# Performance work log

Measured on AMD Instinct MI355X. Metric: run time of the kernel, lower is better.

The kernel has to match this reference:

```python
import jax, jax.numpy as jnp
import numpy as np

D_MODEL = 1024
N_HEADS = 16
D_FF = 4 * D_MODEL
CTX = 2048
EPS = 1e-5


def setup_inputs() -> dict:
    key = jax.random.key(0)
    ks = jax.random.split(key, 8)
    s = 0.02
    z = jax.random.normal(ks[0], (2, CTX, D_MODEL), dtype=jnp.float32)
    W_Q = jax.random.normal(ks[1], (D_MODEL, D_MODEL), dtype=jnp.float32) * s
    W_K = jax.random.normal(ks[2], (D_MODEL, D_MODEL), dtype=jnp.float32) * s
    W_V = jax.random.normal(ks[3], (D_MODEL, D_MODEL), dtype=jnp.float32) * s
    W_O = jax.random.normal(ks[4], (D_MODEL, D_MODEL), dtype=jnp.float32) * s
    W_fc = jax.random.normal(ks[5], (D_MODEL, D_FF), dtype=jnp.float32) * s
    W_proj = jax.random.normal(ks[6], (D_FF, D_MODEL), dtype=jnp.float32) * s
    g1 = jnp.ones((D_MODEL,), dtype=jnp.float32)
    g2 = jnp.ones((D_MODEL,), dtype=jnp.float32)
    return {"z": z, "W_Q": W_Q, "W_K": W_K, "W_V": W_V, "W_O": W_O,
            "W_fc": W_fc, "W_proj": W_proj, "g1": g1, "g2": g2}


def rmsnorm(x, gain):
    rms = jnp.sqrt(jnp.sum(x * x, axis=-1, keepdims=True) / x.shape[-1] + EPS)
    return (x / rms) * gain


def gelu_erf(x):
    return x * 0.5 * (1.0 + jax.lax.erf(x / jnp.sqrt(2.0).astype(x.dtype)))


def attention(zn, W_Q, W_K, W_V, W_O):
    B, T, D = zn.shape
    H = N_HEADS
    dh = D // H
    # [B,T,D] -> [B,H,T,dh]
    def split(x):
        return x.reshape(B, T, H, dh).transpose(0, 2, 1, 3)
    Q = split(zn @ W_Q)
    K = split(zn @ W_K)
    V = split(zn @ W_V)
    scores = jnp.einsum('bhtd,bhsd->bhts', Q, K) / jnp.sqrt(jnp.float32(dh))
    causal = jnp.triu(jnp.ones((T, T), dtype=bool), k=1)  # True above diagonal -> masked
    scores = jnp.where(causal[None, None], -jnp.inf, scores)
    weights = jax.nn.softmax(scores, axis=-1)
    ctx = jnp.einsum('bhts,bhsd->bhtd', weights, V)
    ctx = ctx.transpose(0, 2, 1, 3).reshape(B, T, D)
    return ctx @ W_O


def reference(z, W_Q, W_K, W_V, W_O, W_fc, W_proj, g1, g2):
    # pre-norm GPT block: z + attn(norm1(z)); then + ffn(norm2(z))
    z = z + attention(rmsnorm(z, g1), W_Q, W_K, W_V, W_O)
    h = rmsnorm(z, g2)
    ffn = gelu_erf(h @ W_fc) @ W_proj
    return z + ffn
```

## Files before the change

### kernel.cpp

```cpp
#include <hip/hip_runtime.h>
#include <hip/hip_bf16.h>
#include <math.h>


typedef __bf16 bf16x8 __attribute__((ext_vector_type(8)));
typedef float  f32x4  __attribute__((ext_vector_type(4)));

#define MFMA_16x16x32_BF16(A, B, C) __builtin_amdgcn_mfma_f32_16x16x32_bf16((A), (B), (C), 0, 0, 0)

#define GLDS16(g, l) __builtin_amdgcn_global_load_lds( \
    (const __attribute__((address_space(1))) void*)(g), \
    (__attribute__((address_space(3))) void*)(l), 16, 0, 0)

__global__ __launch_bounds__(256) void transconv_all_kernel(
    const float* __restrict__ W_Q, const float* __restrict__ W_K,
    const float* __restrict__ W_V, const float* __restrict__ W_O,
    const float* __restrict__ W_fc, const float* __restrict__ W_proj,
    __bf16* __restrict__ WtQKV, __bf16* __restrict__ WtO,
    __bf16* __restrict__ Wtfc, __bf16* __restrict__ Wtproj)
{
    const int id = blockIdx.x;
    const float* src;
    __bf16* dst;
    int K, N, nx, t;
    if (id < 4096) {
        const int wsel = id >> 10;
        t = id & 1023;
        src = (wsel == 0) ? W_Q : (wsel == 1) ? W_K : (wsel == 2) ? W_V : W_O;
        dst = (wsel < 3) ? (WtQKV + (size_t)wsel * 1048576) : WtO;
        K = 1024; N = 1024; nx = 32;
    } else if (id < 8192) {
        t = id - 4096; src = W_fc; dst = Wtfc; K = 1024; N = 4096; nx = 128;
    } else {
        t = id - 8192; src = W_proj; dst = Wtproj; K = 4096; N = 1024; nx = 32;
    }
    const int n0 = (t % nx) * 32, k0 = (t / nx) * 32;

    __shared__ float tile[32][33];
    const int c = threadIdx.x & 31, r = threadIdx.x >> 5;
#pragma unroll
    for (int i = 0; i < 4; ++i)
        tile[r + 8 * i][c] = src[(size_t)(k0 + r + 8 * i) * N + n0 + c];
    __syncthreads();
#pragma unroll
    for (int i = 0; i < 4; ++i)
        dst[(size_t)(n0 + r + 8 * i) * K + k0 + c] = (__bf16)tile[c][r + 8 * i];
}

__global__ __launch_bounds__(256) void rmsnorm_kernel(
    const float* __restrict__ x, const float* __restrict__ gain,
    __bf16* __restrict__ out)
{
    const int row = blockIdx.x, t = threadIdx.x;
    const float4 v = ((const float4*)(x + (size_t)row * 1024))[t];
    float ss = v.x * v.x + v.y * v.y + v.z * v.z + v.w * v.w;
#pragma unroll
    for (int m = 1; m < 64; m <<= 1) ss += __shfl_xor(ss, m);
    __shared__ float red[4];
    const int wid = t >> 6, lane = t & 63;
    if (lane == 0) red[wid] = ss;
    __syncthreads();
    const float tot = red[0] + red[1] + red[2] + red[3];
    const float inv = rsqrtf(tot * (1.0f / 1024.0f) + 1e-5f);
    const float4 gv = ((const float4*)gain)[t];
    __bf16* o = out + (size_t)row * 1024 + t * 4;
    o[0] = (__bf16)(v.x * inv * gv.x);
    o[1] = (__bf16)(v.y * inv * gv.y);
    o[2] = (__bf16)(v.z * inv * gv.z);
    o[3] = (__bf16)(v.w * inv * gv.w);
}

template <int BM, int BN, int EPI>
__global__ __launch_bounds__(256) void gemm_bf16(
    const __bf16* __restrict__ A, const __bf16* __restrict__ Bt,
    void* __restrict__ outp, const float* __restrict__ res,
    int M, int N, int K)
{
    __shared__ __bf16 As[2][BM * 64];
    __shared__ __bf16 Bs[2][BN * 64];
    const int tid = threadIdx.x;

    const int gx = gridDim.x, nwg = gx * gridDim.y;
    int bid = blockIdx.y * gx + blockIdx.x;
    if ((nwg & 7) == 0) bid = (bid & 7) * (nwg >> 3) + (bid >> 3);
    const int m0 = (bid / gx) * BM, n0 = (bid % gx) * BN;

    const int lane = tid & 63, w = tid >> 6;
    const int wm = w >> 1, wn = w & 1;
    const int lr = lane & 15, g = lane >> 4;
    const int srow = lane >> 3;
    const int scol = ((lane & 7) ^ srow) * 8;
    const int xr8 = lr & 7;

    constexpr int MI = BM / 32, NI = BN / 32;
    f32x4 acc[MI][NI] = {};

    const __bf16* Abase = A + (size_t)m0 * K;
    const __bf16* Bbase = Bt + (size_t)n0 * K;

    auto STAGE = [&](int kb, int buf) {
#pragma unroll
        for (int j = 0; j < BM / 32; ++j) {
            const int s = j * 4 + w;
            GLDS16(Abase + (size_t)(s * 8 + srow) * K + kb + scol, &As[buf][s * 512]);
        }
#pragma unroll
        for (int j = 0; j < BN / 32; ++j) {
            const int s = j * 4 + w;
            GLDS16(Bbase + (size_t)(s * 8 + srow) * K + kb + scol, &Bs[buf][s * 512]);
        }
    };

    const int nt = K >> 6;
    STAGE(0, 0);
    __syncthreads();

    for (int t = 0; t < nt; ++t) {
        const int cur = t & 1;
        if (t + 1 < nt) STAGE((t + 1) << 6, cur ^ 1);

        bf16x8 af[2][MI], bfr[2][NI];
#pragma unroll
        for (int kk = 0; kk < 2; ++kk) {
#pragma unroll
            for (int i = 0; i < MI; ++i)
                af[kk][i] = *(const bf16x8*)
                    &As[cur][(wm * (BM / 2) + i * 16 + lr) * 64 + (((kk * 4 + g) ^ xr8) << 3)];
#pragma unroll
            for (int i = 0; i < NI; ++i)
                bfr[kk][i] = *(const bf16x8*)
                    &Bs[cur][(wn * (BN / 2) + i * 16 + lr) * 64 + (((kk * 4 + g) ^ xr8) << 3)];
        }
#pragma unroll
        for (int kk = 0; kk < 2; ++kk)
#pragma unroll
            for (int mi = 0; mi < MI; ++mi)
#pragma unroll
                for (int ni = 0; ni < NI; ++ni)
                    acc[mi][ni] = MFMA_16x16x32_BF16(af[kk][mi], bfr[kk][ni], acc[mi][ni]);
        if (t + 1 < nt) __syncthreads();
    }

#pragma unroll
    for (int mi = 0; mi < MI; ++mi)
#pragma unroll
        for (int ni = 0; ni < NI; ++ni) {
            const int colg = n0 + wn * (BN / 2) + ni * 16 + lr;
#pragma unroll
            for (int r = 0; r < 4; ++r) {
                const int rowg = m0 + wm * (BM / 2) + mi * 16 + 4 * g + r;
                const float v = acc[mi][ni][r];
                if constexpr (EPI == 1) {
                    const size_t idx = (size_t)rowg * N + colg;
                    ((float*)outp)[idx] = res[idx] + v;
                } else if constexpr (EPI == 2) {
                    const size_t idx = (size_t)rowg * N + colg;
                    ((__bf16*)outp)[idx] =
                        (__bf16)(0.5f * v * (1.0f + erff(v * 0.70710678118654752f)));
                } else if constexpr (EPI == 3) {
                    const size_t idx = (size_t)rowg * N + colg;
                    ((float*)outp)[idx] += v;
                } else {
                    __bf16* base = (__bf16*)outp;
                    const int seg = colg >> 10;
                    const int cg = colg & 1023;
                    if (seg < 2) {
                        base[(size_t)seg * 4194304 + (size_t)rowg * 1024 + cg] = (__bf16)v;
                    } else {
                        const int tt = rowg & 2047;
                        const int r32 = tt & 31;
                        const int p = ((r32 & 12) << 1) | ((r32 >> 2) & 4) | (r32 & 3);
                        base[8388608 +
                             ((size_t)((rowg >> 11) * 16 + (cg >> 6)) * 64 + (cg & 63)) * 2048 +
                             ((tt & ~31) | p)] = (__bf16)v;
                    }
                }
            }
        }
}

__global__ __launch_bounds__(256) void attn_kernel(
    const __bf16* __restrict__ Q, const __bf16* __restrict__ Kb,
    const __bf16* __restrict__ Vt, __bf16* __restrict__ ctx)
{
    const int Dm = 1024, T = 2048;
    const int tid = threadIdx.x;
    const int w = tid >> 6, lane = tid & 63;
    const int lr = lane & 15, g = lane >> 4;
    const int bx = blockIdx.x;
    const int qc = bx >> 5, bh = bx & 31, b = bh >> 4, h = bh & 15;
    const int qbase = qc * 64 + w * 16;
    const size_t rowoff = (size_t)b * T;
    const __bf16* Qp = Q + rowoff * Dm + h * 64;
    const __bf16* Kp = Kb + rowoff * Dm + h * 64;
    const __bf16* Vtp = Vt + (size_t)bh * 64 * 2048;

    __shared__ __bf16 Ks[2][64 * 64];
    __shared__ __bf16 Vs[2][64 * 64];

    bf16x8 qf0 = *(const bf16x8*)&Qp[(size_t)(qbase + lr) * Dm + g * 8];
    bf16x8 qf1 = *(const bf16x8*)&Qp[(size_t)(qbase + lr) * Dm + 32 + g * 8];
#pragma unroll
    for (int j = 0; j < 8; ++j) {
        qf0[j] = (__bf16)((float)qf0[j] * 0.125f);
        qf1[j] = (__bf16)((float)qf1[j] * 0.125f);
    }

    const int srow = lane >> 3;
    const int schunk = (lane & 7) ^ srow;

    f32x4 acc[4] = {};
    float m_s = -__builtin_inff(), l_s = 0.0f;
    const int nsteps = qc + 1;
    const f32x4 zacc = {0.0f, 0.0f, 0.0f, 0.0f};
    const int xr = (lr & 7) << 3;
    const int qg = qbase + lr;

#pragma unroll
    for (int j = 0; j < 2; ++j) {
        const int row = j * 32 + w * 8 + srow;
        GLDS16(Kp + (size_t)row * Dm + schunk * 8, &Ks[0][(j * 32 + w * 8) * 64]);
        GLDS16(Vtp + (size_t)row * T + schunk * 8, &Vs[0][(j * 32 + w * 8) * 64]);
    }
    __syncthreads();

    for (int t = 0; t < nsteps; ++t) {
        const int kvb = t * 64, cur = t & 1;
        if (t + 1 < nsteps) {
#pragma unroll
            for (int j = 0; j < 2; ++j) {
                const int row = j * 32 + w * 8 + srow;
                GLDS16(Kp + (size_t)(kvb + 64 + row) * Dm + schunk * 8,
                       &Ks[cur ^ 1][(j * 32 + w * 8) * 64]);
                GLDS16(Vtp + (size_t)row * T + kvb + 64 + schunk * 8,
                       &Vs[cur ^ 1][(j * 32 + w * 8) * 64]);
            }
        }

        float sv[4][4];
#pragma unroll
        for (int s4 = 0; s4 < 4; ++s4) {
            const int kv0 = kvb + s4 * 16;
            if (kv0 <= qbase + 15) {
                const int row = s4 * 16 + lr;
                const bf16x8 kfa = *(const bf16x8*)&Ks[cur][row * 64 + ((g * 8) ^ xr)];
                const bf16x8 kfb = *(const bf16x8*)&Ks[cur][row * 64 + ((32 + g * 8) ^ xr)];
                f32x4 st = MFMA_16x16x32_BF16(kfa, qf0, zacc);
                st = MFMA_16x16x32_BF16(kfb, qf1, st);
                const bool domask = (kv0 + 15 > qbase);
#pragma unroll
                for (int r = 0; r < 4; ++r) {
                    float x = st[r];
                    if (domask && (kv0 + 4 * g + r > qg)) x = -__builtin_inff();
                    sv[s4][r] = x;
                }
            } else {
#pragma unroll
                for (int r = 0; r < 4; ++r) sv[s4][r] = -__builtin_inff();
            }
        }

        float tm = sv[0][0];
#pragma unroll
        for (int s4 = 0; s4 < 4; ++s4)
#pragma unroll
            for (int r = 0; r < 4; ++r) tm = fmaxf(tm, sv[s4][r]);
        tm = fmaxf(tm, __shfl_xor(tm, 16));
        tm = fmaxf(tm, __shfl_xor(tm, 32));

        float m_use = m_s;
        if (!__all(tm - m_s <= 8.0f)) {
            m_use = fmaxf(m_s, tm);
            const float corr = __expf(m_s - m_use);
            l_s *= corr;
            float cr[4];
#pragma unroll
            for (int r = 0; r < 4; ++r) cr[r] = __shfl(corr, 4 * g + r);
#pragma unroll
            for (int ct = 0; ct < 4; ++ct) {
                acc[ct][0] *= cr[0]; acc[ct][1] *= cr[1];
                acc[ct][2] *= cr[2]; acc[ct][3] *= cr[3];
            }
            m_s = m_use;
        }

        float rs = 0.0f;
#pragma unroll
        for (int s4 = 0; s4 < 4; ++s4)
#pragma unroll
            for (int r = 0; r < 4; ++r) {
                sv[s4][r] = __expf(sv[s4][r] - m_use);
                rs += sv[s4][r];
            }
        rs += __shfl_xor(rs, 16);
        rs += __shfl_xor(rs, 32);
        l_s += rs;

        bf16x8 pa0, pa1;
#pragma unroll
        for (int r = 0; r < 4; ++r) {
            pa0[r] = (__bf16)sv[0][r];
            pa0[4 + r] = (__bf16)sv[1][r];
            pa1[r] = (__bf16)sv[2][r];
            pa1[4 + r] = (__bf16)sv[3][r];
        }
        const bool liveB = (kvb + 32 <= qbase + 15);
#pragma unroll
        for (int ct = 0; ct < 4; ++ct) {
            const __bf16* vrow = &Vs[cur][(ct * 16 + lr) * 64];
            const bf16x8 vf = *(const bf16x8*)&vrow[(8 * g) ^ xr];
            acc[ct] = MFMA_16x16x32_BF16(pa0, vf, acc[ct]);
            if (liveB) {
                const bf16x8 vf2 = *(const bf16x8*)&vrow[(32 + 8 * g) ^ xr];
                acc[ct] = MFMA_16x16x32_BF16(pa1, vf2, acc[ct]);
            }
        }
        __syncthreads();
    }

    float dn[4];
#pragma unroll
    for (int r = 0; r < 4; ++r) dn[r] = __shfl(l_s, 4 * g + r);
#pragma unroll
    for (int ct = 0; ct < 4; ++ct)
#pragma unroll
        for (int r = 0; r < 4; ++r)
            ctx[(rowoff + qbase + 4 * g + r) * Dm + h * 64 + ct * 16 + lr] =
                (__bf16)(acc[ct][r] / dn[r]);
}

extern "C" void kernel_launch(void* const* d_in, const int* in_sizes, int n_in,
                              void* d_out, int out_size, void* d_ws, size_t ws_size,
                              hipStream_t stream)
{
    (void)in_sizes; (void)n_in; (void)out_size; (void)ws_size;
    const float* z      = (const float*)d_in[0];
    const float* W_Q    = (const float*)d_in[1];
    const float* W_K    = (const float*)d_in[2];
    const float* W_V    = (const float*)d_in[3];
    const float* W_O    = (const float*)d_in[4];
    const float* W_fc   = (const float*)d_in[5];
    const float* W_proj = (const float*)d_in[6];
    const float* g1     = (const float*)d_in[7];
    const float* g2     = (const float*)d_in[8];
    float* out = (float*)d_out;

    char* ws = (char*)d_ws;
    const size_t MB = (size_t)1 << 20;
    __bf16* WtQKV  = (__bf16*)(ws + 0 * MB);
    __bf16* WtO    = (__bf16*)(ws + 6 * MB);
    __bf16* Wtfc   = (__bf16*)(ws + 8 * MB);
    __bf16* Wtproj = (__bf16*)(ws + 16 * MB);
    __bf16* zn     = (__bf16*)(ws + 24 * MB);
    __bf16* Qb     = (__bf16*)(ws + 32 * MB);
    __bf16* Kbuf   = (__bf16*)(ws + 40 * MB);
    __bf16* Vtb    = (__bf16*)(ws + 48 * MB);
    __bf16* ffn1   = (__bf16*)(ws + 40 * MB);
    __bf16* ctx    = zn;
    __bf16* hb     = Qb;

    const int Tt = 2048, Dm = 1024, Bb = 2, M = Bb * Tt, DFF = 4096;
    const dim3 blk256(256);

    transconv_all_kernel<<<12288, blk256, 0, stream>>>(
        W_Q, W_K, W_V, W_O, W_fc, W_proj, WtQKV, WtO, Wtfc, Wtproj);

    rmsnorm_kernel<<<M, blk256, 0, stream>>>(z, g1, zn);

    gemm_bf16<128, 128, 4><<<dim3(24, 32), blk256, 0, stream>>>(
        zn, WtQKV, Qb, nullptr, M, 3072, Dm);

    attn_kernel<<<1024, blk256, 0, stream>>>(Qb, Kbuf, Vtb, ctx);

    gemm_bf16<128, 64, 1><<<dim3(16, 32), blk256, 0, stream>>>(
        ctx, WtO, out, z, M, Dm, Dm);

    rmsnorm_kernel<<<M, blk256, 0, stream>>>(out, g2, hb);

    gemm_bf16<128, 128, 2><<<dim3(32, 32), blk256, 0, stream>>>(
        hb, Wtfc, ffn1, nullptr, M, DFF, Dm);

    gemm_bf16<128, 64, 3><<<dim3(16, 32), blk256, 0, stream>>>(
        ffn1, Wtproj, out, nullptr, M, Dm, DFF);
}
```

Baseline: 275.6 us.

## Triple-buffer GEMM and attention K/V staging with vmcnt waits and priority hints

Both the GEMM and attention kernels move from double to triple-buffered LDS staging. They prefetch two tiles ahead and replace the trailing __syncthreads with an explicit s_waitcnt vmcnt plus a single barrier per iteration, so that global loads overlap more with MFMA work. MFMA sections are wrapped in s_setprio hints. Attention folds log2(e) into the Q scale to use exp2f, raises the lazy-rescale threshold to match, and uses a reciprocal multiply for normalization. The QKV and FC GEMMs switch to 128x64 tiles, trading more LDS per block and smaller tiles for more workgroups.

```diff
diff --git a/kernel.cpp b/kernel.cpp
--- a/kernel.cpp
+++ b/kernel.cpp
@@ -76,8 +76,8 @@
     void* __restrict__ outp, const float* __restrict__ res,
     int M, int N, int K)
 {
-    __shared__ __bf16 As[2][BM * 64];
-    __shared__ __bf16 Bs[2][BN * 64];
+    __shared__ __bf16 As[3][BM * 64];
+    __shared__ __bf16 Bs[3][BN * 64];
     const int tid = threadIdx.x;
 
     const int gx = gridDim.x, nwg = gx * gridDim.y;
@@ -93,12 +93,15 @@
     const int xr8 = lr & 7;
 
     constexpr int MI = BM / 32, NI = BN / 32;
+    constexpr int LCNT = BM / 32 + BN / 32;
     f32x4 acc[MI][NI] = {};
 
     const __bf16* Abase = A + (size_t)m0 * K;
     const __bf16* Bbase = Bt + (size_t)n0 * K;
 
-    auto STAGE = [&](int kb, int buf) {
+    auto STAGE = [&](int t) {
+        const int buf = t % 3;
+        const int kb = t << 6;
 #pragma unroll
         for (int j = 0; j < BM / 32; ++j) {
             const int s = j * 4 + w;
@@ -112,13 +115,17 @@
     };
 
     const int nt = K >> 6;
-    STAGE(0, 0);
-    __syncthreads();
+    STAGE(0);
+    if (nt > 1) STAGE(1);
 
     for (int t = 0; t < nt; ++t) {
-        const int cur = t & 1;
-        if (t + 1 < nt) STAGE((t + 1) << 6, cur ^ 1);
-
+        if (t + 1 < nt) asm volatile("s_waitcnt vmcnt(%0)" :: "i"(LCNT) : "memory");
+        else            asm volatile("s_waitcnt vmcnt(0)" ::: "memory");
+        __builtin_amdgcn_s_barrier();
+        asm volatile("" ::: "memory");
+        if (t + 2 < nt) STAGE(t + 2);
+
+        const int cur = t % 3;
         bf16x8 af[2][MI], bfr[2][NI];
 #pragma unroll
         for (int kk = 0; kk < 2; ++kk) {
@@ -131,6 +138,7 @@
                 bfr[kk][i] = *(const bf16x8*)
                     &Bs[cur][(wn * (BN / 2) + i * 16 + lr) * 64 + (((kk * 4 + g) ^ xr8) << 3)];
         }
+        __builtin_amdgcn_s_setprio(1);
 #pragma unroll
         for (int kk = 0; kk < 2; ++kk)
 #pragma unroll
@@ -138,7 +146,7 @@
 #pragma unroll
                 for (int ni = 0; ni < NI; ++ni)
                     acc[mi][ni] = MFMA_16x16x32_BF16(af[kk][mi], bfr[kk][ni], acc[mi][ni]);
-        if (t + 1 < nt) __syncthreads();
+        __builtin_amdgcn_s_setprio(0);
     }
 
 #pragma unroll
@@ -195,19 +203,31 @@
     const __bf16* Kp = Kb + rowoff * Dm + h * 64;
     const __bf16* Vtp = Vt + (size_t)bh * 64 * 2048;
 
-    __shared__ __bf16 Ks[2][64 * 64];
-    __shared__ __bf16 Vs[2][64 * 64];
+    __shared__ __bf16 Ks[3][64 * 64];
+    __shared__ __bf16 Vs[3][64 * 64];
 
     bf16x8 qf0 = *(const bf16x8*)&Qp[(size_t)(qbase + lr) * Dm + g * 8];
     bf16x8 qf1 = *(const bf16x8*)&Qp[(size_t)(qbase + lr) * Dm + 32 + g * 8];
+    const float qsc = 0.125f * 1.44269504088896340736f;
 #pragma unroll
     for (int j = 0; j < 8; ++j) {
-        qf0[j] = (__bf16)((float)qf0[j] * 0.125f);
-        qf1[j] = (__bf16)((float)qf1[j] * 0.125f);
+        qf0[j] = (__bf16)((float)qf0[j] * qsc);
+        qf1[j] = (__bf16)((float)qf1[j] * qsc);
     }
 
     const int srow = lane >> 3;
     const int schunk = (lane & 7) ^ srow;
+
+    auto STAGE = [&](int t) {
+        const int buf = t % 3;
+        const int kb = t << 6;
+#pragma unroll
+        for (int j = 0; j < 2; ++j) {
+            const int row = j * 32 + w * 8 + srow;
+            GLDS16(Kp + (size_t)(kb + row) * Dm + schunk * 8, &Ks[buf][(j * 32 + w * 8) * 64]);
+            GLDS16(Vtp + (size_t)row * T + kb + schunk * 8, &Vs[buf][(j * 32 + w * 8) * 64]);
+        }
+    };
 
     f32x4 acc[4] = {};
     float m_s = -__builtin_inff(), l_s = 0.0f;
@@ -216,26 +236,17 @@
     const int xr = (lr & 7) << 3;
     const int qg = qbase + lr;
 
-#pragma unroll
-    for (int j = 0; j < 2; ++j) {
-        const int row = j * 32 + w * 8 + srow;
-        GLDS16(Kp + (size_t)row * Dm + schunk * 8, &Ks[0][(j * 32 + w * 8) * 64]);
-        GLDS16(Vtp + (size_t)row * T + schunk * 8, &Vs[0][(j * 32 + w * 8) * 64]);
-    }
-    __syncthreads();
+    STAGE(0);
+    if (nsteps > 1) STAGE(1);
 
     for (int t = 0; t < nsteps; ++t) {
-        const int kvb = t * 64, cur = t & 1;
-        if (t + 1 < nsteps) {
-#pragma unroll
-            for (int j = 0; j < 2; ++j) {
-                const int row = j * 32 + w * 8 + srow;
-                GLDS16(Kp + (size_t)(kvb + 64 + row) * Dm + schunk * 8,
-                       &Ks[cur ^ 1][(j * 32 + w * 8) * 64]);
-                GLDS16(Vtp + (size_t)row * T + kvb + 64 + schunk * 8,
-                       &Vs[cur ^ 1][(j * 32 + w * 8) * 64]);
-            }
-        }
+        if (t + 1 < nsteps) asm volatile("s_waitcnt vmcnt(4)" ::: "memory");
+        else                asm volatile("s_waitcnt vmcnt(0)" ::: "memory");
+        __builtin_amdgcn_s_barrier();
+        asm volatile("" ::: "memory");
+        if (t + 2 < nsteps) STAGE(t + 2);
+
+        const int kvb = t * 64, cur = t % 3;
 
         float sv[4][4];
 #pragma unroll
@@ -245,8 +256,10 @@
                 const int row = s4 * 16 + lr;
                 const bf16x8 kfa = *(const bf16x8*)&Ks[cur][row * 64 + ((g * 8) ^ xr)];
                 const bf16x8 kfb = *(const bf16x8*)&Ks[cur][row * 64 + ((32 + g * 8) ^ xr)];
+                __builtin_amdgcn_s_setprio(1);
                 f32x4 st = MFMA_16x16x32_BF16(kfa, qf0, zacc);
                 st = MFMA_16x16x32_BF16(kfb, qf1, st);
+                __builtin_amdgcn_s_setprio(0);
                 const bool domask = (kv0 + 15 > qbase);
 #pragma unroll
                 for (int r = 0; r < 4; ++r) {
@@ -269,9 +282,9 @@
         tm = fmaxf(tm, __shfl_xor(tm, 32));
 
         float m_use = m_s;
-        if (!__all(tm - m_s <= 8.0f)) {
+        if (!__all(tm - m_s <= 11.5f)) {
             m_use = fmaxf(m_s, tm);
-            const float corr = __expf(m_s - m_use);
+            const float corr = exp2f(m_s - m_use);
             l_s *= corr;
             float cr[4];
 #pragma unroll
@@ -289,7 +302,7 @@
         for (int s4 = 0; s4 < 4; ++s4)
 #pragma unroll
             for (int r = 0; r < 4; ++r) {
-                sv[s4][r] = __expf(sv[s4][r] - m_use);
+                sv[s4][r] = exp2f(sv[s4][r] - m_use);
                 rs += sv[s4][r];
             }
         rs += __shfl_xor(rs, 16);
@@ -305,6 +318,7 @@
             pa1[4 + r] = (__bf16)sv[3][r];
         }
         const bool liveB = (kvb + 32 <= qbase + 15);
+        __builtin_amdgcn_s_setprio(1);
 #pragma unroll
         for (int ct = 0; ct < 4; ++ct) {
             const __bf16* vrow = &Vs[cur][(ct * 16 + lr) * 64];
@@ -315,18 +329,19 @@
                 acc[ct] = MFMA_16x16x32_BF16(pa1, vf2, acc[ct]);
             }
         }
-        __syncthreads();
+        __builtin_amdgcn_s_setprio(0);
     }
 
+    const float il = __builtin_amdgcn_rcpf(l_s);
     float dn[4];
 #pragma unroll
-    for (int r = 0; r < 4; ++r) dn[r] = __shfl(l_s, 4 * g + r);
+    for (int r = 0; r < 4; ++r) dn[r] = __shfl(il, 4 * g + r);
 #pragma unroll
     for (int ct = 0; ct < 4; ++ct)
 #pragma unroll
         for (int r = 0; r < 4; ++r)
             ctx[(rowoff + qbase + 4 * g + r) * Dm + h * 64 + ct * 16 + lr] =
-                (__bf16)(acc[ct][r] / dn[r]);
+                (__bf16)(acc[ct][r] * dn[r]);
 }
 
 extern "C" void kernel_launch(void* const* d_in, const int* in_sizes, int n_in,
@@ -367,7 +382,7 @@
 
     rmsnorm_kernel<<<M, blk256, 0, stream>>>(z, g1, zn);
 
-    gemm_bf16<128, 128, 4><<<dim3(24, 32), blk256, 0, stream>>>(
+    gemm_bf16<128, 64, 4><<<dim3(48, 32), blk256, 0, stream>>>(
         zn, WtQKV, Qb, nullptr, M, 3072, Dm);
 
     attn_kernel<<<1024, blk256, 0, stream>>>(Qb, Kbuf, Vtb, ctx);
@@ -377,7 +392,7 @@
 
     rmsnorm_kernel<<<M, blk256, 0, stream>>>(out, g2, hb);
 
-    gemm_bf16<128, 128, 2><<<dim3(32, 32), blk256, 0, stream>>>(
+    gemm_bf16<128, 64, 2><<<dim3(64, 32), blk256, 0, stream>>>(
         hb, Wtfc, ffn1, nullptr, M, DFF, Dm);
 
     gemm_bf16<128, 64, 3><<<dim3(16, 32), blk256, 0, stream>>>(
```

Measured after the change: 315.8 us. 14.6% more time.
